# Kernel optimization log

Measured on AMD Instinct MI355X. Metric: run time of the kernel, lower is better.

The kernel has to match this reference:

```python
import jax, jax.numpy as jnp
import numpy as np

B, N, C = 2, 2048, 1024
H = 16
D = C // H  # head dim = 64


def setup_inputs() -> dict:
    key = jax.random.key(0)
    ks = jax.random.split(key, 11)
    s = 1.0 / np.sqrt(C)
    inp = {
        "q": jax.random.normal(ks[0], (B, N, C), jnp.float32),
        "k": jax.random.normal(ks[1], (B, N, C), jnp.float32),
        "v": jax.random.normal(ks[2], (B, N, C), jnp.float32),
        # Linear params (kernel shape [in, out], as in flax)
        "Wq": jax.random.normal(ks[3], (C, C), jnp.float32) * s,
        "bq": jnp.zeros((C,), jnp.float32),
        "Wk": jax.random.normal(ks[4], (C, C), jnp.float32) * s,
        "bk": jnp.zeros((C,), jnp.float32),
        "Wv": jax.random.normal(ks[5], (C, C), jnp.float32) * s,
        "bv": jnp.zeros((C,), jnp.float32),
        "Wo": jax.random.normal(ks[6], (C, C), jnp.float32) * s,
        "bo": jnp.zeros((C,), jnp.float32),
    }
    return inp


def reference(q, k, v, Wq, bq, Wk, bk, Wv, bv, Wo, bo):
    # QKV projections: (B,N,C) @ (C,C) + bias
    qh = (q @ Wq + bq).reshape(B, N, H, D).transpose(0, 2, 1, 3)  # b h n d
    kh = (k @ Wk + bk).reshape(B, N, H, D).transpose(0, 2, 1, 3)
    vh = (v @ Wv + bv).reshape(B, N, H, D).transpose(0, 2, 1, 3)
    scale = 1.0 / np.sqrt(D)
    attn = jnp.einsum('bhqd,bhkd->bhqk', qh * scale, kh)  # full NxN scores
    attn = jax.nn.softmax(attn, axis=-1)
    out = jnp.einsum('bhqk,bhkd->bhqd', attn, vh)
    out = out.transpose(0, 2, 1, 3).reshape(B, N, C)
    return out @ Wo + bo
```

## Files before the change

kernel.cpp:

```cpp
#include <hip/hip_runtime.h>
#include <hip/hip_bf16.h>
#include <math.h>


typedef __attribute__((ext_vector_type(8))) short bf16x8;
typedef __attribute__((ext_vector_type(4))) short bf16x4;
typedef __attribute__((ext_vector_type(4))) float f32x4;
typedef __attribute__((ext_vector_type(2))) unsigned int u32x2;

__device__ __forceinline__ short f2bf(float f) {
    union { float f; unsigned u; } x; x.f = f;
    unsigned r = x.u + 0x7fffu + ((x.u >> 16) & 1u);
    return (short)(r >> 16);
}

__device__ __forceinline__ unsigned cvt_pk_bf16(float lo, float hi) {
    unsigned r;
    asm volatile("v_cvt_pk_bf16_f32 %0, %1, %2" : "=v"(r) : "v"(lo), "v"(hi));
    return r;
}

__global__ __launch_bounds__(256) void prep_w(const float* __restrict__ Wq,
                                              const float* __restrict__ Wk,
                                              const float* __restrict__ Wv,
                                              const float* __restrict__ Wo,
                                              short* __restrict__ wt) {
    __shared__ float tile[32][33];
    const float* W = blockIdx.z == 0 ? Wq : blockIdx.z == 1 ? Wk
                   : blockIdx.z == 2 ? Wv : Wo;
    short* dst = wt + (size_t)blockIdx.z * 1048576;
    const int bx = blockIdx.x * 32, by = blockIdx.y * 32;
    const int tx = threadIdx.x & 31, ty = threadIdx.x >> 5;
#pragma unroll
    for (int i = 0; i < 32; i += 8)
        tile[ty + i][tx] = W[(size_t)(by + ty + i) * 1024 + bx + tx];
    __syncthreads();
#pragma unroll
    for (int i = 0; i < 32; i += 8)
        dst[(size_t)(bx + ty + i) * 1024 + by + tx] = f2bf(tile[tx][ty + i]);
}

__global__ __launch_bounds__(256) void gemm_qkv(const float* __restrict__ qA,
                                                const float* __restrict__ kA,
                                                const float* __restrict__ vA,
                                                const short* __restrict__ wt,
                                                const float* __restrict__ bq,
                                                const float* __restrict__ bk,
                                                const float* __restrict__ bv,
                                                short* __restrict__ qh,
                                                short* __restrict__ khp,
                                                short* __restrict__ vtp,
                                                float qscale) {
    __shared__ short As[128 * 32];
    __shared__ short Bs[64 * 32];
    const int tid = threadIdx.x;
    const int l = tid & 63, w = tid >> 6;
    const int wr = w >> 1, wc = w & 1;
    const int row16 = l & 15, lg = l >> 4;
    const int m0 = blockIdx.x * 128;
    const int n0 = blockIdx.y * 64;
    const int z = blockIdx.z;

    const float* A = z == 0 ? qA : z == 1 ? kA : vA;
    const short* Wt = wt + (size_t)z * 1048576;
    const float* bias = z == 0 ? bq : z == 1 ? bk : bv;
    const float scale = z == 0 ? qscale : 1.0f;
    short* outp = z == 0 ? qh : z == 1 ? khp : vtp;

    const int ar = tid >> 1, ac = (tid & 1) * 16;
    const int br = tid >> 2, bc = (tid & 3) * 8;

    f32x4 acc[4][2] = {};

    f32x4 x0, x1, x2, x3; bf16x8 bfrag;
    {
        const float* src = A + (size_t)(m0 + ar) * 1024 + ac;
        x0 = ((const f32x4*)src)[0]; x1 = ((const f32x4*)src)[1];
        x2 = ((const f32x4*)src)[2]; x3 = ((const f32x4*)src)[3];
        bfrag = *(const bf16x8*)(Wt + (size_t)(n0 + br) * 1024 + bc);
    }

    for (int t = 0; t < 32; ++t) {
        __syncthreads();
        bf16x8 sa0, sa1;
#pragma unroll
        for (int j = 0; j < 4; ++j) {
            sa0[j] = f2bf(x0[j]); sa0[4 + j] = f2bf(x1[j]);
            sa1[j] = f2bf(x2[j]); sa1[4 + j] = f2bf(x3[j]);
        }
        *(bf16x8*)&As[ar * 32 + ac]     = sa0;
        *(bf16x8*)&As[ar * 32 + ac + 8] = sa1;
        *(bf16x8*)&Bs[br * 32 + bc]     = bfrag;
        __syncthreads();
        if (t < 31) {
            const int k0 = (t + 1) * 32;
            const float* src = A + (size_t)(m0 + ar) * 1024 + k0 + ac;
            x0 = ((const f32x4*)src)[0]; x1 = ((const f32x4*)src)[1];
            x2 = ((const f32x4*)src)[2]; x3 = ((const f32x4*)src)[3];
            bfrag = *(const bf16x8*)(Wt + (size_t)(n0 + br) * 1024 + k0 + bc);
        }
        bf16x8 af[4], bf2[2];
#pragma unroll
        for (int m = 0; m < 4; ++m)
            af[m] = *(const bf16x8*)&As[(wr * 64 + m * 16 + row16) * 32 + lg * 8];
#pragma unroll
        for (int n = 0; n < 2; ++n)
            bf2[n] = *(const bf16x8*)&Bs[(wc * 32 + n * 16 + row16) * 32 + lg * 8];
#pragma unroll
        for (int m = 0; m < 4; ++m)
#pragma unroll
            for (int n = 0; n < 2; ++n)
                acc[m][n] = __builtin_amdgcn_mfma_f32_16x16x32_bf16(af[m], bf2[n], acc[m][n], 0, 0, 0);
    }

#pragma unroll
    for (int n = 0; n < 2; ++n) {
        const int col = n0 + wc * 32 + n * 16 + row16;
        const float bvl = bias[col];
        const int h = col >> 6, d = col & 63;
#pragma unroll
        for (int m = 0; m < 4; ++m) {
#pragma unroll
            for (int r = 0; r < 4; ++r) {
                const int row = m0 + wr * 64 + m * 16 + lg * 4 + r;
                const float val = (acc[m][n][r] + bvl) * scale;
                const int b = row >> 11, nt = row & 2047;
                if (z != 2)
                    outp[(((size_t)(b * 16 + h)) * 2048 + nt) * 64 + d] = f2bf(val);
                else
                    outp[(((size_t)(b * 16 + h)) * 64 + d) * 2048 + nt] = f2bf(val);
            }
        }
    }
}

__global__ __launch_bounds__(256) void gemm_out(const short* __restrict__ Ab,
                                                const short* __restrict__ Wt,
                                                const float* __restrict__ bias,
                                                float* __restrict__ outp) {
    __shared__ short As[128 * 32];
    __shared__ short Bs[64 * 32];
    const int tid = threadIdx.x;
    const int l = tid & 63, w = tid >> 6;
    const int wr = w >> 1, wc = w & 1;
    const int row16 = l & 15, lg = l >> 4;
    const int m0 = blockIdx.x * 128;
    const int n0 = blockIdx.y * 64;

    const int ar = tid >> 1, ac = (tid & 1) * 16;
    const int br = tid >> 2, bc = (tid & 3) * 8;

    f32x4 acc[4][2] = {};

    bf16x8 sa0, sa1, bfrag;
    sa0 = *(const bf16x8*)(Ab + (size_t)(m0 + ar) * 1024 + ac);
    sa1 = *(const bf16x8*)(Ab + (size_t)(m0 + ar) * 1024 + ac + 8);
    bfrag = *(const bf16x8*)(Wt + (size_t)(n0 + br) * 1024 + bc);

    for (int t = 0; t < 32; ++t) {
        __syncthreads();
        *(bf16x8*)&As[ar * 32 + ac]     = sa0;
        *(bf16x8*)&As[ar * 32 + ac + 8] = sa1;
        *(bf16x8*)&Bs[br * 32 + bc]     = bfrag;
        __syncthreads();
        if (t < 31) {
            const int k0 = (t + 1) * 32;
            sa0 = *(const bf16x8*)(Ab + (size_t)(m0 + ar) * 1024 + k0 + ac);
            sa1 = *(const bf16x8*)(Ab + (size_t)(m0 + ar) * 1024 + k0 + ac + 8);
            bfrag = *(const bf16x8*)(Wt + (size_t)(n0 + br) * 1024 + k0 + bc);
        }
        bf16x8 af[4], bf2[2];
#pragma unroll
        for (int m = 0; m < 4; ++m)
            af[m] = *(const bf16x8*)&As[(wr * 64 + m * 16 + row16) * 32 + lg * 8];
#pragma unroll
        for (int n = 0; n < 2; ++n)
            bf2[n] = *(const bf16x8*)&Bs[(wc * 32 + n * 16 + row16) * 32 + lg * 8];
#pragma unroll
        for (int m = 0; m < 4; ++m)
#pragma unroll
            for (int n = 0; n < 2; ++n)
                acc[m][n] = __builtin_amdgcn_mfma_f32_16x16x32_bf16(af[m], bf2[n], acc[m][n], 0, 0, 0);
    }

#pragma unroll
    for (int n = 0; n < 2; ++n) {
        const int col = n0 + wc * 32 + n * 16 + row16;
        const float bvl = bias[col];
#pragma unroll
        for (int m = 0; m < 4; ++m) {
#pragma unroll
            for (int r = 0; r < 4; ++r) {
                const int row = m0 + wr * 64 + m * 16 + lg * 4 + r;
                outp[(size_t)row * 1024 + col] = acc[m][n][r] + bvl;
            }
        }
    }
}

__device__ __forceinline__ void attn_step(int t,
                                          const short* __restrict__ kbase,
                                          const short* __restrict__ vbase,
                                          bf16x8 (&kc)[4][2],
                                          bf16x8 (&vf)[4][2],
                                          bf16x8 (&qf)[2][2], bf16x8 (&pf)[2][2],
                                          f32x4 (&oac)[2][4], f32x4 (&lacc)[2],
                                          const bf16x8& ones,
                                          short* prow0, short* prow1,
                                          int row16, int lg) {
    const int kvn = t * 64;
    const int kvp = ((t + 2) & 31) * 64;
    short* prow[2] = {prow0, prow1};

    f32x4 s[2][4] = {};
#pragma unroll
    for (int kt = 0; kt < 4; ++kt)
#pragma unroll
        for (int kk = 0; kk < 2; ++kk) {
            s[0][kt] = __builtin_amdgcn_mfma_f32_16x16x32_bf16(kc[kt][kk], qf[0][kk], s[0][kt], 0, 0, 0);
            s[1][kt] = __builtin_amdgcn_mfma_f32_16x16x32_bf16(kc[kt][kk], qf[1][kk], s[1][kt], 0, 0, 0);
        }
#pragma unroll
    for (int kt = 0; kt < 4; ++kt)
#pragma unroll
        for (int kk = 0; kk < 2; ++kk)
            kc[kt][kk] = *(const bf16x8*)&kbase[(size_t)(kvp + kt * 16 + row16) * 64 + kk * 32 + lg * 8];

#pragma unroll
    for (int qt = 0; qt < 2; ++qt)
#pragma unroll
        for (int kt = 0; kt < 4; ++kt) {
            u32x2 pk;
            pk.x = cvt_pk_bf16(exp2f(s[qt][kt][0]), exp2f(s[qt][kt][1]));
            pk.y = cvt_pk_bf16(exp2f(s[qt][kt][2]), exp2f(s[qt][kt][3]));
            *(u32x2*)&prow[qt][kt * 16 + lg * 4] = pk;
        }

#pragma unroll
    for (int dt = 0; dt < 4; ++dt)
#pragma unroll
        for (int kk = 0; kk < 2; ++kk) {
            oac[0][dt] = __builtin_amdgcn_mfma_f32_16x16x32_bf16(pf[0][kk], vf[dt][kk], oac[0][dt], 0, 0, 0);
            oac[1][dt] = __builtin_amdgcn_mfma_f32_16x16x32_bf16(pf[1][kk], vf[dt][kk], oac[1][dt], 0, 0, 0);
        }
#pragma unroll
    for (int qt = 0; qt < 2; ++qt)
#pragma unroll
        for (int kk = 0; kk < 2; ++kk)
            lacc[qt] = __builtin_amdgcn_mfma_f32_16x16x32_bf16(pf[qt][kk], ones, lacc[qt], 0, 0, 0);

#pragma unroll
    for (int dt = 0; dt < 4; ++dt)
#pragma unroll
        for (int kk = 0; kk < 2; ++kk)
            vf[dt][kk] = *(const bf16x8*)&vbase[(size_t)(dt * 16 + row16) * 2048 + kvn + kk * 32 + lg * 8];

    asm volatile("s_waitcnt lgkmcnt(0)" ::: "memory");
#pragma unroll
    for (int qt = 0; qt < 2; ++qt)
#pragma unroll
        for (int kk = 0; kk < 2; ++kk)
            pf[qt][kk] = *(const bf16x8*)&prow[qt][kk * 32 + lg * 8];
    asm volatile("" ::: "memory");
}

__global__ __launch_bounds__(256) void attn_kernel(const short* __restrict__ qh,
                                                   const short* __restrict__ kh,
                                                   const short* __restrict__ vt,
                                                   short* __restrict__ aout) {
    __shared__ short Pls[8][16 * 72];

    const int tid = threadIdx.x;
    const int l = tid & 63, w = tid >> 6;
    const int row16 = l & 15, lg = l >> 4;

    const int fid = blockIdx.y * 16 + blockIdx.x;
    const int xcd = fid & 7, slot = fid >> 3;
    const int bh = xcd * 4 + (slot >> 4);
    const int q0 = (slot & 15) * 128 + w * 32;

    const short* kbase = kh + (size_t)bh * 2048 * 64;
    const short* vbase = vt + (size_t)bh * 64 * 2048;

    bf16x8 qf[2][2];
#pragma unroll
    for (int qt = 0; qt < 2; ++qt)
#pragma unroll
        for (int kk = 0; kk < 2; ++kk)
            qf[qt][kk] = *(const bf16x8*)&qh[((size_t)bh * 2048 + q0 + qt * 16 + row16) * 64 + kk * 32 + lg * 8];

    bf16x8 ones;
#pragma unroll
    for (int j = 0; j < 8; ++j) ones[j] = (short)0x3F80;

    f32x4 oac[2][4] = {};
    f32x4 lacc[2] = {};

    short* prow0 = &Pls[w * 2 + 0][row16 * 72];
    short* prow1 = &Pls[w * 2 + 1][row16 * 72];
    short* prow[2] = {prow0, prow1};

    bf16x8 kfA[4][2], kfB[4][2], vf[4][2], pf[2][2];
#pragma unroll
    for (int kt = 0; kt < 4; ++kt)
#pragma unroll
        for (int kk = 0; kk < 2; ++kk) {
            kfA[kt][kk] = *(const bf16x8*)&kbase[(size_t)(kt * 16 + row16) * 64 + kk * 32 + lg * 8];
            kfB[kt][kk] = *(const bf16x8*)&kbase[(size_t)(64 + kt * 16 + row16) * 64 + kk * 32 + lg * 8];
            vf[kt][kk]  = *(const bf16x8*)&vbase[(size_t)(kt * 16 + row16) * 2048 + kk * 32 + lg * 8];
        }

    {
        f32x4 s[2][4] = {};
#pragma unroll
        for (int kt = 0; kt < 4; ++kt)
#pragma unroll
            for (int kk = 0; kk < 2; ++kk) {
                s[0][kt] = __builtin_amdgcn_mfma_f32_16x16x32_bf16(kfA[kt][kk], qf[0][kk], s[0][kt], 0, 0, 0);
                s[1][kt] = __builtin_amdgcn_mfma_f32_16x16x32_bf16(kfA[kt][kk], qf[1][kk], s[1][kt], 0, 0, 0);
            }
#pragma unroll
        for (int kt = 0; kt < 4; ++kt)
#pragma unroll
            for (int kk = 0; kk < 2; ++kk)
                kfA[kt][kk] = *(const bf16x8*)&kbase[(size_t)(128 + kt * 16 + row16) * 64 + kk * 32 + lg * 8];
#pragma unroll
        for (int qt = 0; qt < 2; ++qt)
#pragma unroll
            for (int kt = 0; kt < 4; ++kt) {
                u32x2 pk;
                pk.x = cvt_pk_bf16(exp2f(s[qt][kt][0]), exp2f(s[qt][kt][1]));
                pk.y = cvt_pk_bf16(exp2f(s[qt][kt][2]), exp2f(s[qt][kt][3]));
                *(u32x2*)&prow[qt][kt * 16 + lg * 4] = pk;
            }
        asm volatile("s_waitcnt lgkmcnt(0)" ::: "memory");
#pragma unroll
        for (int qt = 0; qt < 2; ++qt)
#pragma unroll
            for (int kk = 0; kk < 2; ++kk)
                pf[qt][kk] = *(const bf16x8*)&prow[qt][kk * 32 + lg * 8];
        asm volatile("" ::: "memory");
    }

    for (int tt = 1; tt < 31; tt += 2) {
        attn_step(tt,     kbase, vbase, kfB, vf, qf, pf, oac, lacc, ones, prow0, prow1, row16, lg);
        attn_step(tt + 1, kbase, vbase, kfA, vf, qf, pf, oac, lacc, ones, prow0, prow1, row16, lg);
    }
    attn_step(31, kbase, vbase, kfB, vf, qf, pf, oac, lacc, ones, prow0, prow1, row16, lg);

#pragma unroll
    for (int dt = 0; dt < 4; ++dt)
#pragma unroll
        for (int kk = 0; kk < 2; ++kk) {
            oac[0][dt] = __builtin_amdgcn_mfma_f32_16x16x32_bf16(pf[0][kk], vf[dt][kk], oac[0][dt], 0, 0, 0);
            oac[1][dt] = __builtin_amdgcn_mfma_f32_16x16x32_bf16(pf[1][kk], vf[dt][kk], oac[1][dt], 0, 0, 0);
        }
#pragma unroll
    for (int qt = 0; qt < 2; ++qt)
#pragma unroll
        for (int kk = 0; kk < 2; ++kk)
            lacc[qt] = __builtin_amdgcn_mfma_f32_16x16x32_bf16(pf[qt][kk], ones, lacc[qt], 0, 0, 0);

    const int b = bh >> 4, h = bh & 15;
#pragma unroll
    for (int qt = 0; qt < 2; ++qt) {
#pragma unroll
        for (int r = 0; r < 4; ++r) {
            const float iv = 1.f / lacc[qt][r];
            const int qrow = q0 + qt * 16 + lg * 4 + r;
#pragma unroll
            for (int dt = 0; dt < 4; ++dt) {
                const int c = h * 64 + dt * 16 + row16;
                aout[((size_t)b * 2048 + qrow) * 1024 + c] = f2bf(oac[qt][dt][r] * iv);
            }
        }
    }
}

extern "C" void kernel_launch(void* const* d_in, const int* in_sizes, int n_in,
                              void* d_out, int out_size, void* d_ws, size_t ws_size,
                              hipStream_t stream) {
    const float* q  = (const float*)d_in[0];
    const float* k  = (const float*)d_in[1];
    const float* v  = (const float*)d_in[2];
    const float* Wq = (const float*)d_in[3];
    const float* bq = (const float*)d_in[4];
    const float* Wk = (const float*)d_in[5];
    const float* bk = (const float*)d_in[6];
    const float* Wv = (const float*)d_in[7];
    const float* bv = (const float*)d_in[8];
    const float* Wo = (const float*)d_in[9];
    const float* bo = (const float*)d_in[10];

    char* ws = (char*)d_ws;
    short* wt   = (short*)ws;
    short* qh   = (short*)(ws + (8u  << 20));
    short* khp  = (short*)(ws + (16u << 20));
    short* vt   = (short*)(ws + (24u << 20));
    short* aout = (short*)(ws + (32u << 20));

    const float qscale = 0.125f * 1.44269504088896340736f;

    prep_w<<<dim3(32, 32, 4), 256, 0, stream>>>(Wq, Wk, Wv, Wo, wt);
    gemm_qkv<<<dim3(32, 16, 3), 256, 0, stream>>>(q, k, v, wt, bq, bk, bv,
                                                  qh, khp, vt, qscale);
    attn_kernel<<<dim3(16, 32), 256, 0, stream>>>(qh, khp, vt, aout);
    gemm_out<<<dim3(32, 16), 256, 0, stream>>>(aout, wt + 3145728, bo, (float*)d_out);
}
```

Measured before the change: 220.4 us.

## Split attention over the KV sequence in two halves and combine partial sums

```diff
diff --git a/kernel.cpp b/kernel.cpp
--- a/kernel.cpp
+++ b/kernel.cpp
@@ -15,10 +15,22 @@
 }
 
 __device__ __forceinline__ unsigned cvt_pk_bf16(float lo, float hi) {
+    asm("" ::: );
     unsigned r;
-    asm volatile("v_cvt_pk_bf16_f32 %0, %1, %2" : "=v"(r) : "v"(lo), "v"(hi));
+    asm("v_cvt_pk_bf16_f32 %0, %1, %2" : "=v"(r) : "v"(lo), "v"(hi));
     return r;
 }
+
+__device__ __forceinline__ float fast_exp2(float x) {
+#if __has_builtin(__builtin_amdgcn_exp2f)
+    return __builtin_amdgcn_exp2f(x);
+#else
+    return exp2f(x);
+#endif
+}
+
+union BF8U { unsigned u[4]; bf16x8 v; };
+union BF4U { unsigned u[2]; bf16x4 v; };
 
 __global__ __launch_bounds__(256) void prep_w(const float* __restrict__ Wq,
                                               const float* __restrict__ Wk,
@@ -82,14 +94,13 @@
 
     for (int t = 0; t < 32; ++t) {
         __syncthreads();
-        bf16x8 sa0, sa1;
-#pragma unroll
-        for (int j = 0; j < 4; ++j) {
-            sa0[j] = f2bf(x0[j]); sa0[4 + j] = f2bf(x1[j]);
-            sa1[j] = f2bf(x2[j]); sa1[4 + j] = f2bf(x3[j]);
-        }
-        *(bf16x8*)&As[ar * 32 + ac]     = sa0;
-        *(bf16x8*)&As[ar * 32 + ac + 8] = sa1;
+        BF8U u0, u1;
+        u0.u[0] = cvt_pk_bf16(x0[0], x0[1]); u0.u[1] = cvt_pk_bf16(x0[2], x0[3]);
+        u0.u[2] = cvt_pk_bf16(x1[0], x1[1]); u0.u[3] = cvt_pk_bf16(x1[2], x1[3]);
+        u1.u[0] = cvt_pk_bf16(x2[0], x2[1]); u1.u[1] = cvt_pk_bf16(x2[2], x2[3]);
+        u1.u[2] = cvt_pk_bf16(x3[0], x3[1]); u1.u[3] = cvt_pk_bf16(x3[2], x3[3]);
+        *(bf16x8*)&As[ar * 32 + ac]     = u0.v;
+        *(bf16x8*)&As[ar * 32 + ac + 8] = u1.v;
         *(bf16x8*)&Bs[br * 32 + bc]     = bfrag;
         __syncthreads();
         if (t < 31) {
@@ -198,7 +209,7 @@
     }
 }
 
-__device__ __forceinline__ void attn_step(int t,
+__device__ __forceinline__ void attn_step(int t, int b0, int mask,
                                           const short* __restrict__ kbase,
                                           const short* __restrict__ vbase,
                                           bf16x8 (&kc)[4][2],
@@ -209,7 +220,7 @@
                                           short* prow0, short* prow1,
                                           int row16, int lg) {
     const int kvn = t * 64;
-    const int kvp = ((t + 2) & 31) * 64;
+    const int kvp = (b0 + ((t + 2 - b0) & mask)) * 64;
     short* prow[2] = {prow0, prow1};
 
     f32x4 s[2][4] = {};
@@ -231,8 +242,8 @@
 #pragma unroll
         for (int kt = 0; kt < 4; ++kt) {
             u32x2 pk;
-            pk.x = cvt_pk_bf16(exp2f(s[qt][kt][0]), exp2f(s[qt][kt][1]));
-            pk.y = cvt_pk_bf16(exp2f(s[qt][kt][2]), exp2f(s[qt][kt][3]));
+            pk.x = cvt_pk_bf16(fast_exp2(s[qt][kt][0]), fast_exp2(s[qt][kt][1]));
+            pk.y = cvt_pk_bf16(fast_exp2(s[qt][kt][2]), fast_exp2(s[qt][kt][3]));
             *(u32x2*)&prow[qt][kt * 16 + lg * 4] = pk;
         }
 
@@ -264,10 +275,13 @@
     asm volatile("" ::: "memory");
 }
 
+template <int SPLIT>
 __global__ __launch_bounds__(256) void attn_kernel(const short* __restrict__ qh,
                                                    const short* __restrict__ kh,
                                                    const short* __restrict__ vt,
-                                                   short* __restrict__ aout) {
+                                                   short* __restrict__ aout,
+                                                   float* __restrict__ part,
+                                                   float* __restrict__ lpart) {
     __shared__ short Pls[8][16 * 72];
 
     const int tid = threadIdx.x;
@@ -278,6 +292,10 @@
     const int xcd = fid & 7, slot = fid >> 3;
     const int bh = xcd * 4 + (slot >> 4);
     const int q0 = (slot & 15) * 128 + w * 32;
+    const int z = SPLIT ? blockIdx.z : 0;
+    const int b0 = SPLIT ? z * 16 : 0;
+    const int NT = SPLIT ? 16 : 32;
+    const int mask = NT - 1;
 
     const short* kbase = kh + (size_t)bh * 2048 * 64;
     const short* vbase = vt + (size_t)bh * 64 * 2048;
@@ -305,9 +323,9 @@
     for (int kt = 0; kt < 4; ++kt)
 #pragma unroll
         for (int kk = 0; kk < 2; ++kk) {
-            kfA[kt][kk] = *(const bf16x8*)&kbase[(size_t)(kt * 16 + row16) * 64 + kk * 32 + lg * 8];
-            kfB[kt][kk] = *(const bf16x8*)&kbase[(size_t)(64 + kt * 16 + row16) * 64 + kk * 32 + lg * 8];
-            vf[kt][kk]  = *(const bf16x8*)&vbase[(size_t)(kt * 16 + row16) * 2048 + kk * 32 + lg * 8];
+            kfA[kt][kk] = *(const bf16x8*)&kbase[(size_t)((b0 + 0) * 64 + kt * 16 + row16) * 64 + kk * 32 + lg * 8];
+            kfB[kt][kk] = *(const bf16x8*)&kbase[(size_t)((b0 + 1) * 64 + kt * 16 + row16) * 64 + kk * 32 + lg * 8];
+            vf[kt][kk]  = *(const bf16x8*)&vbase[(size_t)(kt * 16 + row16) * 2048 + b0 * 64 + kk * 32 + lg * 8];
         }
 
     {
@@ -323,14 +341,14 @@
         for (int kt = 0; kt < 4; ++kt)
 #pragma unroll
             for (int kk = 0; kk < 2; ++kk)
-                kfA[kt][kk] = *(const bf16x8*)&kbase[(size_t)(128 + kt * 16 + row16) * 64 + kk * 32 + lg * 8];
+                kfA[kt][kk] = *(const bf16x8*)&kbase[(size_t)((b0 + 2) * 64 + kt * 16 + row16) * 64 + kk * 32 + lg * 8];
 #pragma unroll
         for (int qt = 0; qt < 2; ++qt)
 #pragma unroll
             for (int kt = 0; kt < 4; ++kt) {
                 u32x2 pk;
-                pk.x = cvt_pk_bf16(exp2f(s[qt][kt][0]), exp2f(s[qt][kt][1]));
-                pk.y = cvt_pk_bf16(exp2f(s[qt][kt][2]), exp2f(s[qt][kt][3]));
+                pk.x = cvt_pk_bf16(fast_exp2(s[qt][kt][0]), fast_exp2(s[qt][kt][1]));
+                pk.y = cvt_pk_bf16(fast_exp2(s[qt][kt][2]), fast_exp2(s[qt][kt][3]));
                 *(u32x2*)&prow[qt][kt * 16 + lg * 4] = pk;
             }
         asm volatile("s_waitcnt lgkmcnt(0)" ::: "memory");
@@ -342,11 +360,11 @@
         asm volatile("" ::: "memory");
     }
 
-    for (int tt = 1; tt < 31; tt += 2) {
-        attn_step(tt,     kbase, vbase, kfB, vf, qf, pf, oac, lacc, ones, prow0, prow1, row16, lg);
-        attn_step(tt + 1, kbase, vbase, kfA, vf, qf, pf, oac, lacc, ones, prow0, prow1, row16, lg);
-    }
-    attn_step(31, kbase, vbase, kfB, vf, qf, pf, oac, lacc, ones, prow0, prow1, row16, lg);
+    for (int tt = b0 + 1; tt < b0 + NT - 1; tt += 2) {
+        attn_step(tt,     b0, mask, kbase, vbase, kfB, vf, qf, pf, oac, lacc, ones, prow0, prow1, row16, lg);
+        attn_step(tt + 1, b0, mask, kbase, vbase, kfA, vf, qf, pf, oac, lacc, ones, prow0, prow1, row16, lg);
+    }
+    attn_step(b0 + NT - 1, b0, mask, kbase, vbase, kfB, vf, qf, pf, oac, lacc, ones, prow0, prow1, row16, lg);
 
 #pragma unroll
     for (int dt = 0; dt < 4; ++dt)
@@ -361,20 +379,60 @@
         for (int kk = 0; kk < 2; ++kk)
             lacc[qt] = __builtin_amdgcn_mfma_f32_16x16x32_bf16(pf[qt][kk], ones, lacc[qt], 0, 0, 0);
 
+    if constexpr (SPLIT) {
+        float* pb = part + (size_t)z * 4194304 + (size_t)bh * 2048 * 64;
+        float* lb = lpart + (size_t)z * 65536 + (size_t)bh * 2048;
+#pragma unroll
+        for (int qt = 0; qt < 2; ++qt)
+#pragma unroll
+            for (int r = 0; r < 4; ++r) {
+                const int qrow = q0 + qt * 16 + lg * 4 + r;
+#pragma unroll
+                for (int dt = 0; dt < 4; ++dt)
+                    pb[(size_t)qrow * 64 + dt * 16 + row16] = oac[qt][dt][r];
+            }
+        if (row16 == 0) {
+#pragma unroll
+            for (int qt = 0; qt < 2; ++qt)
+#pragma unroll
+                for (int r = 0; r < 4; ++r)
+                    lb[q0 + qt * 16 + lg * 4 + r] = lacc[qt][r];
+        }
+    } else {
+        const int b = bh >> 4, h = bh & 15;
+#pragma unroll
+        for (int qt = 0; qt < 2; ++qt) {
+#pragma unroll
+            for (int r = 0; r < 4; ++r) {
+                const float iv = 1.f / lacc[qt][r];
+                const int qrow = q0 + qt * 16 + lg * 4 + r;
+#pragma unroll
+                for (int dt = 0; dt < 4; ++dt) {
+                    const int c = h * 64 + dt * 16 + row16;
+                    aout[((size_t)b * 2048 + qrow) * 1024 + c] = f2bf(oac[qt][dt][r] * iv);
+                }
+            }
+        }
+    }
+}
+
+__global__ __launch_bounds__(256) void attn_combine(const float* __restrict__ part,
+                                                    const float* __restrict__ lpart,
+                                                    short* __restrict__ aout) {
+    const int g = blockIdx.x * 256 + threadIdx.x;
+    const int c4 = g & 15;
+    const int q  = (g >> 4) & 2047;
+    const int bh = g >> 15;
+    const size_t po = ((size_t)bh * 2048 + q) * 64 + c4 * 4;
+    f32x4 p0 = *(const f32x4*)&part[po];
+    f32x4 p1 = *(const f32x4*)&part[4194304 + po];
+    const float lsum = lpart[bh * 2048 + q] + lpart[65536 + bh * 2048 + q];
+    const float iv = 1.f / lsum;
+    BF4U o;
+    o.u[0] = cvt_pk_bf16((p0[0] + p1[0]) * iv, (p0[1] + p1[1]) * iv);
+    o.u[1] = cvt_pk_bf16((p0[2] + p1[2]) * iv, (p0[3] + p1[3]) * iv);
     const int b = bh >> 4, h = bh & 15;
-#pragma unroll
-    for (int qt = 0; qt < 2; ++qt) {
-#pragma unroll
-        for (int r = 0; r < 4; ++r) {
-            const float iv = 1.f / lacc[qt][r];
-            const int qrow = q0 + qt * 16 + lg * 4 + r;
-#pragma unroll
-            for (int dt = 0; dt < 4; ++dt) {
-                const int c = h * 64 + dt * 16 + row16;
-                aout[((size_t)b * 2048 + qrow) * 1024 + c] = f2bf(oac[qt][dt][r] * iv);
-            }
-        }
-    }
+    *(bf16x4*)&aout[((size_t)b * 2048 + q) * 1024 + h * 64 + c4 * 4] = o.v;
 }
 
 extern "C" void kernel_launch(void* const* d_in, const int* in_sizes, int n_in,
@@ -398,12 +456,20 @@
     short* khp  = (short*)(ws + (16u << 20));
     short* vt   = (short*)(ws + (24u << 20));
     short* aout = (short*)(ws + (32u << 20));
+    float* part = (float*)(ws + (40u << 20));
+    float* lprt = (float*)(ws + (72u << 20));
 
     const float qscale = 0.125f * 1.44269504088896340736f;
+    const bool split = ws_size >= (76ull << 20);
 
     prep_w<<<dim3(32, 32, 4), 256, 0, stream>>>(Wq, Wk, Wv, Wo, wt);
     gemm_qkv<<<dim3(32, 16, 3), 256, 0, stream>>>(q, k, v, wt, bq, bk, bv,
                                                   qh, khp, vt, qscale);
-    attn_kernel<<<dim3(16, 32), 256, 0, stream>>>(qh, khp, vt, aout);
+    if (split) {
+        attn_kernel<1><<<dim3(16, 32, 2), 256, 0, stream>>>(qh, khp, vt, aout, part, lprt);
+        attn_combine<<<4096, 256, 0, stream>>>(part, lprt, aout);
+    } else {
+        attn_kernel<0><<<dim3(16, 32), 256, 0, stream>>>(qh, khp, vt, aout, nullptr, nullptr);
+    }
     gemm_out<<<dim3(32, 16), 256, 0, stream>>>(aout, wt + 3145728, bo, (float*)d_out);
 }
```

Result: no change. 224.3 us (+1.7%).
